# Kernel optimization log

Hardware: AMD Instinct MI355X
Metric: run time of the kernel (lower is better)

## Reference

```python
import jax, jax.numpy as jnp
import numpy as np
from jax import lax

B, LE, LD = 16, 512, 256
D, H, DFF = 512, 8, 2048
ENC_IN, DEC_IN, MARK, CO = 7, 7, 4, 7
NE, ND = 3, 2
TOPK = int((D // H) * 0.25)  # 16, from ProbSparseMultiheadAttention


def layer_norm(x, p):
    m = jnp.mean(x, -1, keepdims=True)
    v = jnp.mean((x - m) ** 2, -1, keepdims=True)
    return (x - m) / jnp.sqrt(v + 1e-5) * p[0] + p[1]


def attn(q, k, v, W, b, mask=None, topk=None):
    # W: [4, D, D] (q,k,v,o), b: [4, D]
    Bq, Lq, _ = q.shape
    dk = D // H
    Q = (q @ W[0] + b[0]).reshape(Bq, Lq, H, dk)
    K = (k @ W[1] + b[1]).reshape(Bq, -1, H, dk)
    V = (v @ W[2] + b[2]).reshape(Bq, -1, H, dk)
    s = jnp.einsum('bqhd,bkhd->bhqk', Q, K) / jnp.sqrt(jnp.float32(dk))
    if mask is not None:
        s = s + mask * (-1e9)
    if topk is not None:
        # ProbSparse: keep only top-k key scores per query before softmax
        kth = lax.top_k(s, topk)[0][..., -1:]
        s = jnp.where(s >= kth, s, -1e9)
    w = jax.nn.softmax(s, axis=-1)
    o = jnp.einsum('bhqk,bkhd->bqhd', w, V).reshape(Bq, Lq, D)
    return o @ W[3] + b[3]


def conv_distill(x, w, cb, g, bb):
    # x: [B, L, D]; circular-pad conv1d(k=3, pad=2) + BN(batch stats) + ELU + maxpool(k3,s2,p1)
    xc = jnp.transpose(x, (0, 2, 1))
    xp = jnp.pad(xc, ((0, 0), (0, 0), (2, 2)), mode='wrap')
    y = lax.conv_general_dilated(xp, w, (1,), 'VALID', dimension_numbers=('NCH', 'OIH', 'NCH')) + cb[None, :, None]
    m = jnp.mean(y, (0, 2), keepdims=True)
    v = jnp.var(y, (0, 2), keepdims=True)
    y = (y - m) / jnp.sqrt(v + 1e-5) * g[None, :, None] + bb[None, :, None]
    y = jax.nn.elu(y)
    y = lax.reduce_window(y, -jnp.inf, lax.max, (1, 1, 3), (1, 1, 2), ((0, 0), (0, 0), (1, 1)))
    return jnp.transpose(y, (0, 2, 1))


def setup_inputs() -> dict:
    key = jax.random.key(0)
    ks = iter(jax.random.split(key, 64))
    def nrm(shape, s=0.02):
        return jax.random.normal(next(ks), shape, dtype=jnp.float32) * s
    def ln_p(*lead):
        return jnp.stack([jnp.ones(lead + (D,), jnp.float32), jnp.zeros(lead + (D,), jnp.float32)], axis=len(lead))
    return {
        'x_enc': nrm((B, LE, ENC_IN), 1.0),
        'x_mark_enc': nrm((B, LE, MARK), 1.0),
        'x_dec': nrm((B, LD, DEC_IN), 1.0),
        'x_mark_dec': nrm((B, LD, MARK), 1.0),
        'enc_vw': nrm((ENC_IN, D)), 'enc_vb': jnp.zeros((D,)),
        'enc_mw': nrm((MARK, D)), 'enc_mb': jnp.zeros((D,)),
        'dec_vw': nrm((DEC_IN, D)), 'dec_vb': jnp.zeros((D,)),
        'dec_mw': nrm((MARK, D)), 'dec_mb': jnp.zeros((D,)),
        'eW': nrm((NE, 4, D, D)), 'eb': jnp.zeros((NE, 4, D)),
        'effw1': nrm((NE, D, DFF)), 'effb1': jnp.zeros((NE, DFF)),
        'effw2': nrm((NE, DFF, D)), 'effb2': jnp.zeros((NE, D)),
        'eln1': ln_p(NE), 'eln2': ln_p(NE),
        'cw': nrm((NE - 1, D, D, 3)), 'cb': jnp.zeros((NE - 1, D)),
        'cbn_g': jnp.ones((NE - 1, D)), 'cbn_b': jnp.zeros((NE - 1, D)),
        'enc_norm': ln_p(),
        'dsW': nrm((ND, 4, D, D)), 'dsb': jnp.zeros((ND, 4, D)),
        'dcW': nrm((ND, 4, D, D)), 'dcb': jnp.zeros((ND, 4, D)),
        'dffw1': nrm((ND, D, DFF)), 'dffb1': jnp.zeros((ND, DFF)),
        'dffw2': nrm((ND, DFF, D)), 'dffb2': jnp.zeros((ND, D)),
        'dln': ln_p(ND, 3),
        'dec_norm': ln_p(),
        'fcw': nrm((D, CO)), 'fcb': jnp.zeros((CO,)),
    }


def reference(x_enc, x_mark_enc, x_dec, x_mark_dec, enc_vw, enc_vb, enc_mw, enc_mb,
              dec_vw, dec_vb, dec_mw, dec_mb, eW, eb, effw1, effb1, effw2, effb2,
              eln1, eln2, cw, cb, cbn_g, cbn_b, enc_norm, dsW, dsb, dcW, dcb,
              dffw1, dffb1, dffw2, dffb2, dln, dec_norm, fcw, fcb):
    # embedding: value projection + temporal-mark projection
    x = x_enc @ enc_vw + enc_vb + x_mark_enc @ enc_mw + enc_mb
    # encoder: ProbSparse attn layers with conv distillation after the first NE-1
    for i in range(NE):
        a = attn(x, x, x, eW[i], eb[i], topk=TOPK)
        x = layer_norm(x + a, eln1[i])
        f = jax.nn.relu(x @ effw1[i] + effb1[i]) @ effw2[i] + effb2[i]
        x = layer_norm(x + f, eln2[i])
        if i < NE - 1:
            x = conv_distill(x, cw[i], cb[i], cbn_g[i], cbn_b[i])
    mem = layer_norm(x, enc_norm)
    # decoder
    y = x_dec @ dec_vw + dec_vb + x_mark_dec @ dec_mw + dec_mb
    cmask = jnp.triu(jnp.ones((LD, LD), jnp.float32), 1)[None, None]
    for i in range(ND):
        a = attn(y, y, y, dsW[i], dsb[i], mask=cmask)
        y = layer_norm(y + a, dln[i, 0])
        a = attn(y, mem, mem, dcW[i], dcb[i])
        y = layer_norm(y + a, dln[i, 1])
        f = jax.nn.relu(y @ dffw1[i] + dffb1[i]) @ dffw2[i] + dffb2[i]
        y = layer_norm(y + f, dln[i, 2])
    y = layer_norm(y, dec_norm)
    return y @ fcw + fcb
```

## Files before the change

kernel.cpp:

```cpp
#include <hip/hip_runtime.h>
#include <hip/hip_bf16.h>


#define DM 512
#define DK 64

using bf16 = __hip_bfloat16;
typedef short s8v __attribute__((ext_vector_type(8)));
typedef float f4v __attribute__((ext_vector_type(4)));

__device__ inline float b2f(bf16 x) { return __bfloat162float(x); }
__device__ inline float u2f(unsigned short u) { return __uint_as_float((unsigned)u << 16); }

__device__ inline float ldw(const void* p, unsigned i, int f) {
    return f ? b2f(((const bf16*)p)[i]) : ((const float*)p)[i];
}

__device__ inline unsigned f2ord(float s) {
    unsigned u = __float_as_uint(s);
    return u ^ ((unsigned)((int)u >> 31) | 0x80000000u);
}

__device__ inline int popc_lt(unsigned long long m) {
    return (int)__builtin_amdgcn_mbcnt_hi((unsigned)(m >> 32),
            __builtin_amdgcn_mbcnt_lo((unsigned)m, 0u));
}

__device__ inline void gl_lds16(const short* g, short* l) {
    __builtin_amdgcn_global_load_lds(
        (const __attribute__((address_space(1))) unsigned int*)g,
        (__attribute__((address_space(3))) unsigned int*)l,
        16, 0, 0);
}

__global__ __launch_bounds__(256) void sniff_k(const unsigned* __restrict__ x, int nwords,
                                               int* __restrict__ flag) {
    __shared__ int red[4];
    const int t = threadIdx.x;
    int c = 0;
    for (int i = t; i < nwords; i += 256) c += ((x[i] & 0x7F80u) == 0x3F80u) ? 1 : 0;
    #pragma unroll
    for (int o = 32; o > 0; o >>= 1) c += __shfl_down(c, o);
    __syncthreads();
    if ((t & 63) == 0) red[t >> 6] = c;
    __syncthreads();
    if (t == 0) flag[0] = (red[0] + red[1] + red[2] + red[3] > nwords / 20) ? 1 : 0;
}

__device__ inline float block_sum256(float v, float* red) {
    #pragma unroll
    for (int o = 32; o > 0; o >>= 1) v += __shfl_down(v, o);
    __syncthreads();
    if ((threadIdx.x & 63) == 0) red[threadIdx.x >> 6] = v;
    __syncthreads();
    return red[0] + red[1] + red[2] + red[3];
}

__global__ __launch_bounds__(256) void embed_k(
    const void* __restrict__ xv, const void* __restrict__ vw, const void* __restrict__ vb,
    const void* __restrict__ xm, const void* __restrict__ mw, const void* __restrict__ mb,
    bf16* __restrict__ Out, int rows, int Cv, int Cm, const int* __restrict__ flagp)
{
    const int f = *flagp;
    int i = blockIdx.x * 256 + threadIdx.x;
    if (i >= rows * DM) return;
    const int r = i >> 9, d = i & 511;
    float acc = ldw(vb, d, f) + ldw(mb, d, f);
    for (int c = 0; c < Cv; ++c) acc += ldw(xv, r * Cv + c, f) * ldw(vw, c * DM + d, f);
    for (int c = 0; c < Cm; ++c) acc += ldw(xm, r * Cm + c, f) * ldw(mw, c * DM + d, f);
    Out[i] = __float2bfloat16(acc);
}

__global__ __launch_bounds__(256) void transp_k(
    const void* __restrict__ W, unsigned off, unsigned zstride, bf16* __restrict__ out,
    int K, int N, const int* __restrict__ flagp)
{
    __shared__ float tile[32][33];
    const int f = *flagp;
    const unsigned zo = blockIdx.z * zstride;
    const int t = threadIdx.x;
    const int tx = t & 31, ty = t >> 5;
    const int n0 = blockIdx.x * 32, k0 = blockIdx.y * 32;
    #pragma unroll
    for (int i = 0; i < 4; ++i)
        tile[ty + 8 * i][tx] = ldw(W, off + zo + (unsigned)(k0 + ty + 8 * i) * N + n0 + tx, f);
    __syncthreads();
    #pragma unroll
    for (int i = 0; i < 4; ++i)
        out[(size_t)zo + (size_t)(n0 + ty + 8 * i) * K + k0 + tx] = __float2bfloat16(tile[tx][ty + 8 * i]);
}

template<bool G3, bool RELU>
__global__ __launch_bounds__(256) void mgemm_k(
    const short* __restrict__ A, const int* __restrict__ ridx,
    const short* __restrict__ Wt,
    const void* __restrict__ bias, unsigned boff0,
    bf16* __restrict__ C, int M, int N, int K, int lda, int ldc,
    const int* __restrict__ flagp)
{
    __shared__ short As[2][128 * 32];
    __shared__ short Ws[2][128 * 32];
    const int t = threadIdx.x;
    const int bm = blockIdx.y * 128, bn = blockIdx.x * 128;
    const int lane = t & 63, wave = t >> 6;
    const int mbase = (wave >> 1) * 64, nbase = (wave & 1) * 64;
    const int l15 = lane & 15, quad = lane >> 4;
    const int lrow = lane >> 2, lk = (lane & 3) * 8;

    f4v acc[4][4] = {};

    auto stage = [&](int buf, int k0) {
        #pragma unroll
        for (int j = 0; j < 2; ++j) {
            const int rb = wave * 32 + j * 16;
            const int row = bm + rb + lrow;
            const int rowc = row < M ? row : M - 1;
            const short* g;
            if (G3) {
                const int r = ridx[(k0 >> 9) * M + rowc];
                g = A + (size_t)r * lda + (k0 & 511) + lk;
            } else {
                g = A + (size_t)rowc * lda + k0 + lk;
            }
            gl_lds16(g, &As[buf][rb * 32]);
        }
        #pragma unroll
        for (int j = 0; j < 2; ++j) {
            const int nb = wave * 32 + j * 16;
            gl_lds16(Wt + (size_t)(bn + nb + lrow) * K + k0 + lk, &Ws[buf][nb * 32]);
        }
    };

    const int nt = K >> 5;
    stage(0, 0);
    __syncthreads();
    for (int it = 0; it < nt; ++it) {
        if (it + 1 < nt) stage((it + 1) & 1, (it + 1) << 5);
        const int cb = it & 1;
        s8v af[4], bfv[4];
        #pragma unroll
        for (int i = 0; i < 4; ++i) {
            af[i]  = *(const s8v*)&As[cb][(mbase + i * 16 + l15) * 32 + quad * 8];
            bfv[i] = *(const s8v*)&Ws[cb][(nbase + i * 16 + l15) * 32 + quad * 8];
        }
        #pragma unroll
        for (int mi = 0; mi < 4; ++mi)
            #pragma unroll
            for (int ni = 0; ni < 4; ++ni)
                acc[mi][ni] = __builtin_amdgcn_mfma_f32_16x16x32_bf16(
                    af[mi], bfv[ni], acc[mi][ni], 0, 0, 0);
        if (it + 1 < nt) __syncthreads();
    }

    const int f = *flagp;
    float bv[4];
    #pragma unroll
    for (int ni = 0; ni < 4; ++ni)
        bv[ni] = ldw(bias, boff0 + (unsigned)(bn + nbase + ni * 16 + l15), f);

    #pragma unroll
    for (int mi = 0; mi < 4; ++mi) {
        #pragma unroll
        for (int r = 0; r < 4; ++r) {
            const int row = bm + mbase + mi * 16 + quad * 4 + r;
            if (row < M) {
                #pragma unroll
                for (int ni = 0; ni < 4; ++ni) {
                    float o = acc[mi][ni][r] + bv[ni];
                    if (RELU) o = fmaxf(o, 0.f);
                    C[(size_t)row * ldc + bn + nbase + ni * 16 + l15] = __float2bfloat16(o);
                }
            }
        }
    }
}

template<bool G3, bool RELU>
__global__ __launch_bounds__(256) void mgemm64_k(
    const short* __restrict__ A, const int* __restrict__ ridx,
    const short* __restrict__ Wt,
    const void* __restrict__ bias, unsigned boff0,
    bf16* __restrict__ C, int M, int N, int K, int lda, int ldc,
    const int* __restrict__ flagp)
{
    __shared__ short As[2][64 * 32];
    __shared__ short Ws[2][64 * 32];
    const int t = threadIdx.x;
    const int bm = blockIdx.y * 64, bn = blockIdx.x * 64;
    const int lane = t & 63, wave = t >> 6;
    const int mbase = (wave >> 1) * 32, nbase = (wave & 1) * 32;
    const int l15 = lane & 15, quad = lane >> 4;
    const int lrow = lane >> 2, lk = (lane & 3) * 8;

    f4v acc[2][2] = {};

    auto stage = [&](int buf, int k0) {
        {
            const int rb = wave * 16;
            const int row = bm + rb + lrow;
            const int rowc = row < M ? row : M - 1;
            const short* g;
            if (G3) {
                const int r = ridx[(k0 >> 9) * M + rowc];
                g = A + (size_t)r * lda + (k0 & 511) + lk;
            } else {
                g = A + (size_t)rowc * lda + k0 + lk;
            }
            gl_lds16(g, &As[buf][rb * 32]);
        }
        {
            const int nb = wave * 16;
            gl_lds16(Wt + (size_t)(bn + nb + lrow) * K + k0 + lk, &Ws[buf][nb * 32]);
        }
    };

    const int nt = K >> 5;
    stage(0, 0);
    __syncthreads();
    for (int it = 0; it < nt; ++it) {
        if (it + 1 < nt) stage((it + 1) & 1, (it + 1) << 5);
        const int cb = it & 1;
        s8v af[2], bfv[2];
        #pragma unroll
        for (int i = 0; i < 2; ++i) {
            af[i]  = *(const s8v*)&As[cb][(mbase + i * 16 + l15) * 32 + quad * 8];
            bfv[i] = *(const s8v*)&Ws[cb][(nbase + i * 16 + l15) * 32 + quad * 8];
        }
        #pragma unroll
        for (int mi = 0; mi < 2; ++mi)
            #pragma unroll
            for (int ni = 0; ni < 2; ++ni)
                acc[mi][ni] = __builtin_amdgcn_mfma_f32_16x16x32_bf16(
                    af[mi], bfv[ni], acc[mi][ni], 0, 0, 0);
        if (it + 1 < nt) __syncthreads();
    }

    const int f = *flagp;
    float bv[2];
    #pragma unroll
    for (int ni = 0; ni < 2; ++ni)
        bv[ni] = ldw(bias, boff0 + (unsigned)(bn + nbase + ni * 16 + l15), f);

    #pragma unroll
    for (int mi = 0; mi < 2; ++mi) {
        #pragma unroll
        for (int r = 0; r < 4; ++r) {
            const int row = bm + mbase + mi * 16 + quad * 4 + r;
            if (row < M) {
                #pragma unroll
                for (int ni = 0; ni < 2; ++ni) {
                    float o = acc[mi][ni][r] + bv[ni];
                    if (RELU) o = fmaxf(o, 0.f);
                    C[(size_t)row * ldc + bn + nbase + ni * 16 + l15] = __float2bfloat16(o);
                }
            }
        }
    }
}

template<int MODE>
__global__ __launch_bounds__(512, 8) void fattn_k(
    bf16* __restrict__ q, const bf16* __restrict__ k, const bf16* __restrict__ v,
    int ldq, int ldkv, int Lq, int Lk)
{
    __shared__ short Qs[16 * 72];
    __shared__ float S[16 * 516];
    __shared__ int   PC[16][16];
    __shared__ float PE[16][16];

    const int t = threadIdx.x;
    const int q0 = blockIdx.x * 16, h = blockIdx.y, b = blockIdx.z;
    const int lane = t & 63, wave = t >> 6;
    const int l15 = lane & 15, quad = lane >> 4;

    const int qv = (Lq - q0) < 16 ? (Lq - q0) : 16;

    const bf16* Kbase = k + (size_t)b * Lk * ldkv + h * DK;
    const bf16* Vbase = v + (size_t)b * Lk * ldkv + h * DK;
    bf16* Qbase = q + (size_t)(b * Lq + q0) * ldq + h * DK;

    const int kmax = (MODE == 1) ? (q0 + 16 < Lk ? q0 + 16 : Lk) : Lk;
    const int ntile = (kmax + 63) >> 6;
    const int kpad = ntile << 6;
    const int nchunk = kpad >> 4;

    {
        const int qr = t >> 5;
        const int qsrc = qr < qv ? qr : qv - 1;
        *(ushort2*)&Qs[qr * 72 + (t & 31) * 2] =
            *(const ushort2*)(Qbase + (size_t)qsrc * ldq + (t & 31) * 2);
    }
    __syncthreads();

    {
        const s8v a0 = *(const s8v*)&Qs[l15 * 72 + quad * 8];
        const s8v a1 = *(const s8v*)&Qs[l15 * 72 + 32 + quad * 8];
        int c = wave;
        s8v b0, b1;
        if (c < nchunk) {
            int srow = c * 16 + l15; if (srow >= Lk) srow = Lk - 1;
            const bf16* kp = Kbase + (size_t)srow * ldkv + quad * 8;
            b0 = *(const s8v*)kp;
            b1 = *(const s8v*)(kp + 32);
        }
        while (c < nchunk) {
            const int cn = c + 8;
            s8v n0, n1;
            if (cn < nchunk) {
                int srow = cn * 16 + l15; if (srow >= Lk) srow = Lk - 1;
                const bf16* kp = Kbase + (size_t)srow * ldkv + quad * 8;
                n0 = *(const s8v*)kp;
                n1 = *(const s8v*)(kp + 32);
            }
            f4v acc = {0.f, 0.f, 0.f, 0.f};
            acc = __builtin_amdgcn_mfma_f32_16x16x32_bf16(a0, b0, acc, 0, 0, 0);
            acc = __builtin_amdgcn_mfma_f32_16x16x32_bf16(a1, b1, acc, 0, 0, 0);
            const int colg = c * 16 + l15;
            #pragma unroll
            for (int r = 0; r < 4; ++r) {
                const int qrow = quad * 4 + r;
                float s = acc[r] * 0.125f;
                if (colg >= Lk) s = -1e9f;
                if (MODE == 1 && colg > q0 + qrow) s = -1e9f;
                S[qrow * 516 + colg] = s;
            }
            b0 = n0; b1 = n1; c = cn;
        }
    }
    __syncthreads();

    const int rowA = wave, rowB = wave + 8;
    float aA = 0.f, aB = 0.f;
    float invA, invB;
    if (MODE == 0) {
        unsigned keyA[8], keyB[8];
        #pragma unroll
        for (int j = 0; j < 8; ++j) {
            const int col = lane + 64 * j;
            const bool ok = col < kpad;
            keyA[j] = ok ? ((f2ord(S[rowA * 516 + col]) & 0xFFFFFE00u) | (unsigned)col) : 0u;
            keyB[j] = ok ? ((f2ord(S[rowB * 516 + col]) & 0xFFFFFE00u) | (unsigned)col) : 0u;
        }
        unsigned kmA = keyA[0], kmB = keyB[0];
        #pragma unroll
        for (int j = 1; j < 8; ++j) {
            kmA = kmA > keyA[j] ? kmA : keyA[j];
            kmB = kmB > keyB[j] ? kmB : keyB[j];
        }
        #pragma unroll
        for (int off = 1; off < 64; off <<= 1) {
            const unsigned oA = __shfl_xor(kmA, off);
            const unsigned oB = __shfl_xor(kmB, off);
            kmA = kmA > oA ? kmA : oA;
            kmB = kmB > oB ? kmB : oB;
        }
        const float mrA = S[rowA * 516 + (int)(kmA & 511u)];
        const float mrB = S[rowB * 516 + (int)(kmB & 511u)];

        unsigned TA = 0u, TB = 0u;
        bool dA = false, dB = false;
        for (int bbit = 31; bbit >= 0; --bbit) {
            if (!dA) {
                const unsigned T2 = TA | (1u << bbit);
                int c = 0;
                #pragma unroll
                for (int j = 0; j < 8; ++j)
                    c += (int)__popcll(__ballot(keyA[j] >= T2));
                if (c >= 16) { TA = T2; dA = (c == 16); }
            }
            if (!dB) {
                const unsigned T2 = TB | (1u << bbit);
                int c = 0;
                #pragma unroll
                for (int j = 0; j < 8; ++j)
                    c += (int)__popcll(__ballot(keyB[j] >= T2));
                if (c >= 16) { TB = T2; dB = (c == 16); }
            }
            if (dA && dB) break;
        }

        int cntA = 0, cntB = 0;
        #pragma unroll
        for (int j = 0; j < 8; ++j) {
            const bool sA = keyA[j] >= TA;
            const unsigned long long balA = __ballot(sA);
            if (sA) {
                const int p = cntA + popc_lt(balA);
                const int col = (int)(keyA[j] & 511u);
                PC[rowA][p] = col;
                PE[rowA][p] = expf(S[rowA * 516 + col] - mrA);
            }
            cntA += (int)__popcll(balA);
            const bool sB = keyB[j] >= TB;
            const unsigned long long balB = __ballot(sB);
            if (sB) {
                const int p = cntB + popc_lt(balB);
                const int col = (int)(keyB[j] & 511u);
                PC[rowB][p] = col;
                PE[rowB][p] = expf(S[rowB * 516 + col] - mrB);
            }
            cntB += (int)__popcll(balB);
        }

        float denA = 0.f, denB = 0.f;
        #pragma unroll
        for (int it = 0; it < 16; ++it) {
            const int cA = PC[rowA][it];
            const float eA = PE[rowA][it];
            denA += eA;
            aA += eA * b2f(Vbase[(size_t)cA * ldkv + lane]);
            const int cB = PC[rowB][it];
            const float eB = PE[rowB][it];
            denB += eB;
            aB += eB * b2f(Vbase[(size_t)cB * ldkv + lane]);
        }
        invA = 1.f / denA;
        invB = 1.f / denB;
    } else {
        float lvA = -INFINITY, lvB = -INFINITY;
        #pragma unroll
        for (int j = 0; j < 8; ++j) {
            const int col = lane + 64 * j;
            if (col < kpad) {
                lvA = fmaxf(lvA, S[rowA * 516 + col]);
                lvB = fmaxf(lvB, S[rowB * 516 + col]);
            }
        }
        #pragma unroll
        for (int off = 1; off < 64; off <<= 1) {
            lvA = fmaxf(lvA, __shfl_xor(lvA, off));
            lvB = fmaxf(lvB, __shfl_xor(lvB, off));
        }
        float pA = 0.f, pB = 0.f;
        #pragma unroll
        for (int j = 0; j < 8; ++j) {
            const int col = lane + 64 * j;
            if (col < kpad) {
                const float wA = expf(S[rowA * 516 + col] - lvA);
                const float wB = expf(S[rowB * 516 + col] - lvB);
                S[rowA * 516 + col] = wA;
                S[rowB * 516 + col] = wB;
                pA += wA; pB += wB;
            }
        }
        #pragma unroll
        for (int off = 1; off < 64; off <<= 1) {
            pA += __shfl_xor(pA, off);
            pB += __shfl_xor(pB, off);
        }
        invA = 1.f / pA;
        invB = 1.f / pB;
        #pragma unroll 8
        for (int k2 = 0; k2 < kmax; ++k2) {
            const float vv = b2f(Vbase[(size_t)k2 * ldkv + lane]);
            aA += S[rowA * 516 + k2] * vv;
            aB += S[rowB * 516 + k2] * vv;
        }
    }
    if (rowA < qv)
        Qbase[(size_t)rowA * ldq + lane] = __float2bfloat16(aA * invA);
    if (rowB < qv)
        Qbase[(size_t)rowB * ldq + lane] = __float2bfloat16(aB * invB);
}

__global__ __launch_bounds__(256) void ln_off_k(
    const bf16* __restrict__ X, const bf16* __restrict__ R,
    const void* __restrict__ gb, unsigned goff,
    bf16* __restrict__ Out, const int* __restrict__ flagp)
{
    __shared__ float red[4];
    const int f = *flagp;
    const int t = threadIdx.x;
    const size_t base = (size_t)blockIdx.x * DM;
    float v0 = b2f(X[base + t]), v1 = b2f(X[base + t + 256]);
    if (R) { v0 += b2f(R[base + t]); v1 += b2f(R[base + t + 256]); }
    const float mean = block_sum256(v0 + v1, red) * (1.f / 512.f);
    const float d0 = v0 - mean, d1 = v1 - mean;
    const float var = block_sum256(d0 * d0 + d1 * d1, red) * (1.f / 512.f);
    const float rstd = rsqrtf(var + 1e-5f);
    Out[base + t]       = __float2bfloat16(d0 * rstd * ldw(gb, goff + t, f)       + ldw(gb, goff + 512 + t, f));
    Out[base + t + 256] = __float2bfloat16(d1 * rstd * ldw(gb, goff + t + 256, f) + ldw(gb, goff + 768 + t, f));
}

__global__ __launch_bounds__(256) void convw_k(const void* __restrict__ w,
                                               bf16* __restrict__ wt, int total,
                                               const int* __restrict__ flagp) {
    const int f = *flagp;
    int i = blockIdx.x * 256 + threadIdx.x;
    if (i >= total) return;
    const int layer = i / 786432, rem2 = i % 786432;
    const int o = rem2 / 1536, rem = rem2 % 1536;
    const int j = rem >> 9, c = rem & 511;
    wt[i] = __float2bfloat16(ldw(w, (unsigned)layer * 786432u + (unsigned)(o * 512 + c) * 3 + j, f));
}

__global__ __launch_bounds__(256) void convidx_k(int* __restrict__ idx, int Lc, int L, int total) {
    int i = blockIdx.x * 256 + threadIdx.x;
    if (i >= total) return;
    const int j = i / (16 * Lc), mrem = i % (16 * Lc);
    const int b = mrem / Lc, l = mrem % Lc;
    int src = l + j - 2;
    src %= L; if (src < 0) src += L;
    idx[i] = b * L + src;
}

__global__ __launch_bounds__(256) void bnstat1_k(const bf16* __restrict__ Y, float* __restrict__ part, int M) {
    const int t = threadIdx.x;
    float s0 = 0.f, q0 = 0.f, s1 = 0.f, q1 = 0.f;
    for (int r = blockIdx.x; r < M; r += gridDim.x) {
        const ushort2 u = *reinterpret_cast<const ushort2*>(Y + (size_t)r * DM + t * 2);
        const float a = u2f(u.x), c = u2f(u.y);
        s0 += a; q0 += a * a;
        s1 += c; q1 += c * c;
    }
    float* p = part + (size_t)blockIdx.x * 1024;
    p[2 * t] = s0; p[2 * t + 1] = s1;
    p[512 + 2 * t] = q0; p[512 + 2 * t + 1] = q1;
}

__global__ __launch_bounds__(256) void bnstat2_k(const float* __restrict__ part, float* __restrict__ stats,
                                                 int nchunk, int M) {
    const int ch = blockIdx.x * 256 + threadIdx.x;
    if (ch >= 512) return;
    float S = 0.f, Qs = 0.f;
    for (int c = 0; c < nchunk; ++c) { S += part[c * 1024 + ch]; Qs += part[c * 1024 + 512 + ch]; }
    const float mean = S / (float)M;
    const float var = Qs / (float)M - mean * mean;
    stats[ch] = mean;
    stats[512 + ch] = fmaxf(var, 0.f);
}

__global__ __launch_bounds__(256) void bnpool_k(
    const bf16* __restrict__ Yc, const float* __restrict__ stats,
    const void* __restrict__ g, const void* __restrict__ bb, unsigned off,
    bf16* __restrict__ Out, int Lc, int Lout, int total, const int* __restrict__ flagp)
{
    const int f = *flagp;
    int i = blockIdx.x * 256 + threadIdx.x;
    if (i >= total) return;
    const int ch = i & 511;
    const int lp = (i >> 9) % Lout;
    const int b = i / (512 * Lout);
    const float mean = stats[ch], var = stats[512 + ch];
    const float sc = ldw(g, off + ch, f) * rsqrtf(var + 1e-5f);
    const float sh = ldw(bb, off + ch, f) - mean * sc;
    float mx = -INFINITY;
    const int l0 = 2 * lp - 1;
    #pragma unroll
    for (int d = 0; d < 3; ++d) {
        const int l = l0 + d;
        if (l >= 0 && l < Lc) {
            float v = b2f(Yc[((size_t)b * Lc + l) * DM + ch]) * sc + sh;
            v = v > 0.f ? v : expm1f(v);
            mx = fmaxf(mx, v);
        }
    }
    Out[((size_t)b * Lout + lp) * DM + ch] = __float2bfloat16(mx);
}

__global__ __launch_bounds__(256) void fc_k(
    const bf16* __restrict__ Yn, const void* __restrict__ fcw, const void* __restrict__ fcb,
    void* __restrict__ out, int total, const int* __restrict__ flagp)
{
    const int f = *flagp;
    int i = blockIdx.x * 256 + threadIdx.x;
    if (i >= total) return;
    const int r = i / 7, co = i % 7;
    const bf16* yr = Yn + (size_t)r * DM;
    float acc = ldw(fcb, co, f);
    for (int d = 0; d < DM; ++d) acc += b2f(yr[d]) * ldw(fcw, d * 7 + co, f);
    if (f) ((bf16*)out)[i] = __float2bfloat16(acc);
    else   ((float*)out)[i] = acc;
}

extern "C" void kernel_launch(void* const* d_in, const int* in_sizes, int n_in,
                              void* d_out, int out_size, void* d_ws, size_t ws_size,
                              hipStream_t stream)
{
    const void* x_enc      = d_in[0];
    const void* x_mark_enc = d_in[1];
    const void* x_dec      = d_in[2];
    const void* x_mark_dec = d_in[3];
    const void* enc_vw = d_in[4];
    const void* enc_vb = d_in[5];
    const void* enc_mw = d_in[6];
    const void* enc_mb = d_in[7];
    const void* dec_vw = d_in[8];
    const void* dec_vb = d_in[9];
    const void* dec_mw = d_in[10];
    const void* dec_mb = d_in[11];
    const void* eW    = d_in[12];
    const void* ebi   = d_in[13];
    const void* effw1 = d_in[14];
    const void* effb1 = d_in[15];
    const void* effw2 = d_in[16];
    const void* effb2 = d_in[17];
    const void* eln1  = d_in[18];
    const void* eln2  = d_in[19];
    const void* cw    = d_in[20];
    const void* cb    = d_in[21];
    const void* cbn_g = d_in[22];
    const void* cbn_b = d_in[23];
    const void* enc_norm = d_in[24];
    const void* dsW   = d_in[25];
    const void* dsb   = d_in[26];
    const void* dcW   = d_in[27];
    const void* dcb   = d_in[28];
    const void* dffw1 = d_in[29];
    const void* dffb1 = d_in[30];
    const void* dffw2 = d_in[31];
    const void* dffb2 = d_in[32];
    const void* dln   = d_in[33];
    const void* dec_norm = d_in[34];
    const void* fcw   = d_in[35];
    const void* fcb   = d_in[36];

    char* wsp = (char*)d_ws;
    bf16* X    = (bf16*)wsp;
    bf16* QKV  = (bf16*)(wsp + ((size_t)8 << 20));
    bf16* HID  = QKV;
    bf16* OUT  = (bf16*)(wsp + ((size_t)40 << 20));
    bf16* WT   = (bf16*)(wsp + ((size_t)48 << 20));
    int*   IDX0 = (int*)(wsp + ((size_t)88 << 20));
    int*   IDX1 = IDX0 + 24672;
    float* PART = (float*)(wsp + ((size_t)89 << 20));
    float* STATS= (float*)(wsp + ((size_t)89 << 20) + (1 << 18));
    int*   FLAG = (int*)(wsp + ((size_t)89 << 20) + (1 << 18) + 4096);
    bf16* MEMb = X;
    bf16* Yd   = (bf16*)(wsp + (size_t)16 * 130 * 512 * 2);

    bf16* WTE  = WT;
    bf16* EW1T = WT + 3145728;
    bf16* EW2T = WT + 6291456;
    bf16* CWT  = WT + 9437184;
    bf16* DSWt = WT + 11010048;
    bf16* DCWt = WT + 13107200;
    bf16* DW1T = WT + 15204352;
    bf16* DW2T = WT + 17301504;

    auto cdiv = [](int a, int b) { return (a + b - 1) / b; };
    auto gemm = [&](const bf16* A, const bf16* Wt, const void* bias, unsigned boff,
                    bf16* C, int M, int N, int K, int lda, int ldc, bool relu) {
        dim3 g(N / 128, cdiv(M, 128));
        if (relu) mgemm_k<false, true><<<g, 256, 0, stream>>>(
            (const short*)A, nullptr, (const short*)Wt, bias, boff, C, M, N, K, lda, ldc, FLAG);
        else      mgemm_k<false, false><<<g, 256, 0, stream>>>(
            (const short*)A, nullptr, (const short*)Wt, bias, boff, C, M, N, K, lda, ldc, FLAG);
    };
    auto gemm64 = [&](const bf16* A, const bf16* Wt, const void* bias, unsigned boff,
                      bf16* C, int M, int N, int K, int lda, int ldc, bool relu) {
        dim3 g(N / 64, cdiv(M, 64));
        if (relu) mgemm64_k<false, true><<<g, 256, 0, stream>>>(
            (const short*)A, nullptr, (const short*)Wt, bias, boff, C, M, N, K, lda, ldc, FLAG);
        else      mgemm64_k<false, false><<<g, 256, 0, stream>>>(
            (const short*)A, nullptr, (const short*)Wt, bias, boff, C, M, N, K, lda, ldc, FLAG);
    };
    auto transp = [&](const void* W, unsigned zstride, int nz, bf16* out, int K, int N) {
        transp_k<<<dim3(N / 32, K / 32, nz), 256, 0, stream>>>(W, 0u, zstride, out, K, N, FLAG);
    };

    sniff_k<<<1, 256, 0, stream>>>((const unsigned*)x_mark_enc, 16384, FLAG);
    transp(eW,    262144u, 12, WTE,  512, 512);
    transp(effw1, 1048576u, 3, EW1T, 512, 2048);
    transp(effw2, 1048576u, 3, EW2T, 2048, 512);
    convw_k<<<cdiv(1572864, 256), 256, 0, stream>>>(cw, CWT, 1572864, FLAG);
    transp(dsW,   262144u, 8, DSWt, 512, 512);
    transp(dcW,   262144u, 8, DCWt, 512, 512);
    transp(dffw1, 1048576u, 2, DW1T, 512, 2048);
    transp(dffw2, 1048576u, 2, DW2T, 2048, 512);
    convidx_k<<<cdiv(24672, 256), 256, 0, stream>>>(IDX0, 514, 512, 24672);
    convidx_k<<<cdiv(12432, 256), 256, 0, stream>>>(IDX1, 259, 257, 12432);
    embed_k<<<cdiv(16 * 512 * 512, 256), 256, 0, stream>>>(
        x_enc, enc_vw, enc_vb, x_mark_enc, enc_mw, enc_mb, X, 16 * 512, 7, 4, FLAG);

    int L = 512;
    for (int i = 0; i < 3; ++i) {
        const int rows = 16 * L;
        const unsigned b0 = (unsigned)i * 4u * 512u;
        if (i == 0) gemm(X, WTE + (size_t)i * 4 * 262144, ebi, b0, QKV, rows, 1536, 512, 512, 1536, false);
        else      gemm64(X, WTE + (size_t)i * 4 * 262144, ebi, b0, QKV, rows, 1536, 512, 512, 1536, false);
        fattn_k<0><<<dim3(cdiv(L, 16), 8, 16), 512, 0, stream>>>(
            QKV, QKV + 512, QKV + 1024, 1536, 1536, L, L);
        gemm64(QKV, WTE + (size_t)(i * 4 + 3) * 262144, ebi, b0 + 1536u, OUT, rows, 512, 512, 1536, 512, false);
        ln_off_k<<<rows, 256, 0, stream>>>(X, OUT, eln1, (unsigned)i * 1024u, X, FLAG);

        if (i == 0) gemm(X, EW1T + (size_t)i * 1048576, effb1, (unsigned)i * 2048u, HID, rows, 2048, 512, 512, 2048, true);
        else      gemm64(X, EW1T + (size_t)i * 1048576, effb1, (unsigned)i * 2048u, HID, rows, 2048, 512, 512, 2048, true);
        gemm64(HID, EW2T + (size_t)i * 1048576, effb2, (unsigned)i * 512u, OUT, rows, 512, 2048, 2048, 512, false);
        ln_off_k<<<rows, 256, 0, stream>>>(X, OUT, eln2, (unsigned)i * 1024u, X, FLAG);

        if (i < 2) {
            const int Lc = L + 2, Mc = 16 * Lc;
            const int* IDXi = (i == 0) ? IDX0 : IDX1;
            mgemm64_k<true, false><<<dim3(8, cdiv(Mc, 64)), 256, 0, stream>>>(
                (const short*)X, IDXi, (const short*)(CWT + (size_t)i * 786432),
                cb, (unsigned)i * 512u, QKV, Mc, 512, 1536, 512, 512, FLAG);
            bnstat1_k<<<32, 256, 0, stream>>>(QKV, PART, Mc);
            bnstat2_k<<<2, 256, 0, stream>>>(PART, STATS, 32, Mc);
            const int Lout = (L + 1) / 2 + 1;
            const int tot = 16 * Lout * 512;
            bnpool_k<<<cdiv(tot, 256), 256, 0, stream>>>(
                QKV, STATS, cbn_g, cbn_b, (unsigned)i * 512u, X, Lc, Lout, tot, FLAG);
            L = Lout;
        }
    }
    const int Lm = L;
    ln_off_k<<<16 * Lm, 256, 0, stream>>>(X, nullptr, enc_norm, 0u, MEMb, FLAG);

    const int rowsD = 16 * 256;
    embed_k<<<cdiv(rowsD * 512, 256), 256, 0, stream>>>(
        x_dec, dec_vw, dec_vb, x_mark_dec, dec_mw, dec_mb, Yd, rowsD, 7, 4, FLAG);

    bf16* CQ  = QKV;
    bf16* CKV = QKV + (size_t)4096 * 512;
    for (int i = 0; i < 2; ++i) {
        const unsigned b0 = (unsigned)i * 4u * 512u;
        gemm64(Yd, DSWt + (size_t)i * 4 * 262144, dsb, b0, QKV, rowsD, 1536, 512, 512, 1536, false);
        fattn_k<1><<<dim3(16, 8, 16), 512, 0, stream>>>(
            QKV, QKV + 512, QKV + 1024, 1536, 1536, 256, 256);
        gemm64(QKV, DSWt + (size_t)(i * 4 + 3) * 262144, dsb, b0 + 1536u, OUT, rowsD, 512, 512, 1536, 512, false);
        ln_off_k<<<rowsD, 256, 0, stream>>>(Yd, OUT, dln, (unsigned)(i * 3 + 0) * 1024u, Yd, FLAG);

        gemm64(Yd, DCWt + (size_t)i * 4 * 262144, dcb, b0, CQ, rowsD, 512, 512, 512, 512, false);
        gemm64(MEMb, DCWt + (size_t)(i * 4 + 1) * 262144, dcb, b0 + 512u, CKV, 16 * Lm, 1024, 512, 512, 1024, false);
        fattn_k<2><<<dim3(16, 8, 16), 512, 0, stream>>>(
            CQ, CKV, CKV + 512, 512, 1024, 256, Lm);
        gemm64(CQ, DCWt + (size_t)(i * 4 + 3) * 262144, dcb, b0 + 1536u, OUT, rowsD, 512, 512, 512, 512, false);
        ln_off_k<<<rowsD, 256, 0, stream>>>(Yd, OUT, dln, (unsigned)(i * 3 + 1) * 1024u, Yd, FLAG);

        gemm64(Yd, DW1T + (size_t)i * 1048576, dffb1, (unsigned)i * 2048u, HID, rowsD, 2048, 512, 512, 2048, true);
        gemm64(HID, DW2T + (size_t)i * 1048576, dffb2, (unsigned)i * 512u, OUT, rowsD, 512, 2048, 2048, 512, false);
        ln_off_k<<<rowsD, 256, 0, stream>>>(Yd, OUT, dln, (unsigned)(i * 3 + 2) * 1024u, Yd, FLAG);
    }

    ln_off_k<<<rowsD, 256, 0, stream>>>(Yd, nullptr, dec_norm, 0u, OUT, FLAG);
    fc_k<<<cdiv(rowsD * 7, 256), 256, 0, stream>>>(OUT, fcw, fcb, d_out, rowsD * 7, FLAG);
}
```

Measured before the change: 1.451 ms.

## Single-buffer mgemm, remap attention workgroups, unroll and widen BN stats

The 128x128 GEMM drops double-buffered LDS staging and goes back to a single buffer with two barriers per k-step. This halves its LDS use but removes the overlap between loads and MFMA. The attention kernel remaps its linear block index so that consecutive blocks are spread across eight groups, which looks aimed at XCD/L2 locality on MI355X. The BN statistics kernel unrolls its row loop by four and doubles the grid to 64 blocks, so the partial-sum reduction now covers 64 chunks.

```diff
diff --git a/kernel.cpp b/kernel.cpp
--- a/kernel.cpp
+++ b/kernel.cpp
@@ -98,8 +98,8 @@
     bf16* __restrict__ C, int M, int N, int K, int lda, int ldc,
     const int* __restrict__ flagp)
 {
-    __shared__ short As[2][128 * 32];
-    __shared__ short Ws[2][128 * 32];
+    __shared__ short As[128 * 32];
+    __shared__ short Ws[128 * 32];
     const int t = threadIdx.x;
     const int bm = blockIdx.y * 128, bn = blockIdx.x * 128;
     const int lane = t & 63, wave = t >> 6;
@@ -109,7 +109,8 @@
 
     f4v acc[4][4] = {};
 
-    auto stage = [&](int buf, int k0) {
+    for (int k0 = 0; k0 < K; k0 += 32) {
+        __syncthreads();
         #pragma unroll
         for (int j = 0; j < 2; ++j) {
             const int rb = wave * 32 + j * 16;
@@ -122,26 +123,19 @@
             } else {
                 g = A + (size_t)rowc * lda + k0 + lk;
             }
-            gl_lds16(g, &As[buf][rb * 32]);
+            gl_lds16(g, &As[rb * 32]);
         }
         #pragma unroll
         for (int j = 0; j < 2; ++j) {
             const int nb = wave * 32 + j * 16;
-            gl_lds16(Wt + (size_t)(bn + nb + lrow) * K + k0 + lk, &Ws[buf][nb * 32]);
-        }
-    };
-
-    const int nt = K >> 5;
-    stage(0, 0);
-    __syncthreads();
-    for (int it = 0; it < nt; ++it) {
-        if (it + 1 < nt) stage((it + 1) & 1, (it + 1) << 5);
-        const int cb = it & 1;
+            gl_lds16(Wt + (size_t)(bn + nb + lrow) * K + k0 + lk, &Ws[nb * 32]);
+        }
+        __syncthreads();
         s8v af[4], bfv[4];
         #pragma unroll
         for (int i = 0; i < 4; ++i) {
-            af[i]  = *(const s8v*)&As[cb][(mbase + i * 16 + l15) * 32 + quad * 8];
-            bfv[i] = *(const s8v*)&Ws[cb][(nbase + i * 16 + l15) * 32 + quad * 8];
+            af[i]  = *(const s8v*)&As[(mbase + i * 16 + l15) * 32 + quad * 8];
+            bfv[i] = *(const s8v*)&Ws[(nbase + i * 16 + l15) * 32 + quad * 8];
         }
         #pragma unroll
         for (int mi = 0; mi < 4; ++mi)
@@ -149,7 +143,6 @@
             for (int ni = 0; ni < 4; ++ni)
                 acc[mi][ni] = __builtin_amdgcn_mfma_f32_16x16x32_bf16(
                     af[mi], bfv[ni], acc[mi][ni], 0, 0, 0);
-        if (it + 1 < nt) __syncthreads();
     }
 
     const int f = *flagp;
@@ -269,7 +262,14 @@
     __shared__ float PE[16][16];
 
     const int t = threadIdx.x;
-    const int q0 = blockIdx.x * 16, h = blockIdx.y, b = blockIdx.z;
+    const int gx = gridDim.x;
+    const int nwg = gx * 128;
+    const int lin = blockIdx.x + gx * (blockIdx.y + 8 * blockIdx.z);
+    const int id = (lin & 7) * (nwg >> 3) + (lin >> 3);
+    const int q0 = (id % gx) * 16;
+    const int h  = (id / gx) & 7;
+    const int b  = id / (gx * 8);
+
     const int lane = t & 63, wave = t >> 6;
     const int l15 = lane & 15, quad = lane >> 4;
 
@@ -506,8 +506,21 @@
 
 __global__ __launch_bounds__(256) void bnstat1_k(const bf16* __restrict__ Y, float* __restrict__ part, int M) {
     const int t = threadIdx.x;
+    const int g = gridDim.x;
     float s0 = 0.f, q0 = 0.f, s1 = 0.f, q1 = 0.f;
-    for (int r = blockIdx.x; r < M; r += gridDim.x) {
+    int r = blockIdx.x;
+    for (; r + 3 * g < M; r += 4 * g) {
+        const ushort2 u0 = *reinterpret_cast<const ushort2*>(Y + (size_t)r * DM + t * 2);
+        const ushort2 u1 = *reinterpret_cast<const ushort2*>(Y + (size_t)(r + g) * DM + t * 2);
+        const ushort2 u2 = *reinterpret_cast<const ushort2*>(Y + (size_t)(r + 2 * g) * DM + t * 2);
+        const ushort2 u3 = *reinterpret_cast<const ushort2*>(Y + (size_t)(r + 3 * g) * DM + t * 2);
+        float a, c;
+        a = u2f(u0.x); c = u2f(u0.y); s0 += a; q0 += a * a; s1 += c; q1 += c * c;
+        a = u2f(u1.x); c = u2f(u1.y); s0 += a; q0 += a * a; s1 += c; q1 += c * c;
+        a = u2f(u2.x); c = u2f(u2.y); s0 += a; q0 += a * a; s1 += c; q1 += c * c;
+        a = u2f(u3.x); c = u2f(u3.y); s0 += a; q0 += a * a; s1 += c; q1 += c * c;
+    }
+    for (; r < M; r += g) {
         const ushort2 u = *reinterpret_cast<const ushort2*>(Y + (size_t)r * DM + t * 2);
         const float a = u2f(u.x), c = u2f(u.y);
         s0 += a; q0 += a * a;
@@ -695,8 +708,8 @@
             mgemm64_k<true, false><<<dim3(8, cdiv(Mc, 64)), 256, 0, stream>>>(
                 (const short*)X, IDXi, (const short*)(CWT + (size_t)i * 786432),
                 cb, (unsigned)i * 512u, QKV, Mc, 512, 1536, 512, 512, FLAG);
-            bnstat1_k<<<32, 256, 0, stream>>>(QKV, PART, Mc);
-            bnstat2_k<<<2, 256, 0, stream>>>(PART, STATS, 32, Mc);
+            bnstat1_k<<<64, 256, 0, stream>>>(QKV, PART, Mc);
+            bnstat2_k<<<2, 256, 0, stream>>>(PART, STATS, 64, Mc);
             const int Lout = (L + 1) / 2 + 1;
             const int tot = 16 * Lout * 512;
             bnpool_k<<<cdiv(tot, 256), 256, 0, stream>>>(
```

After: 1.367 ms. 5.8% less time.
